# Performance work log

Hardware: AMD Instinct MI355X
Metric: run time of the kernel (lower is better)

The kernel has to match this reference:

```python
import jax, jax.numpy as jnp
import numpy as np

N_NODES = 1024
BATCH = 64
IN_CH = 12        # history steps = GAT feature dim = LSTM sequence length
N_PRED = 12
HEADS = 8
E = 1048576       # edges in the batched graph (avg degree 16)
N = BATCH * N_NODES
K = N_NODES * N_PRED
H1, H2 = 32, 128  # lstm hidden sizes


def setup_inputs() -> dict:
    key = jax.random.key(0)
    ks = jax.random.split(key, 16)
    s = 0.05
    f32 = jnp.float32
    return {
        "x": jax.random.normal(ks[0], (N, IN_CH), f32),
        "edge_index": jax.random.randint(ks[1], (2, E), 0, N, jnp.int32),
        # GATConv params (concat=False -> head-mean, bias of size out_channels)
        "gat_W": jax.random.normal(ks[2], (HEADS * IN_CH, IN_CH), f32) * s,
        "att_src": jax.random.normal(ks[3], (HEADS, IN_CH), f32) * s,
        "att_dst": jax.random.normal(ks[4], (HEADS, IN_CH), f32) * s,
        "gat_bias": jnp.zeros((IN_CH,), f32),
        # LSTM1: input_size = n_nodes, hidden 32 (PyTorch gate order i,f,g,o)
        "lstm1_Wih": jax.random.normal(ks[5], (4 * H1, N_NODES), f32) * s,
        "lstm1_Whh": jax.random.normal(ks[6], (4 * H1, H1), f32) * s,
        "lstm1_bih": jnp.zeros((4 * H1,), f32),
        "lstm1_bhh": jnp.zeros((4 * H1,), f32),
        # LSTM2: input 32 -> hidden 128
        "lstm2_Wih": jax.random.normal(ks[7], (4 * H2, H1), f32) * s,
        "lstm2_Whh": jax.random.normal(ks[8], (4 * H2, H2), f32) * s,
        "lstm2_bih": jnp.zeros((4 * H2,), f32),
        "lstm2_bhh": jnp.zeros((4 * H2,), f32),
        # MLP head
        "lin1_W": jax.random.normal(ks[9], (K // 2, H2), f32) * s,
        "lin1_b": jnp.zeros((K // 2,), f32),
        "lin2_W": jax.random.normal(ks[10], (K, K // 2), f32) * s,
        "lin2_b": jnp.zeros((K,), f32),
    }


def _lstm(xs, Wih, Whh, bih, bhh, hid):
    # xs: [T, B, in]; returns all hidden states [T, B, hid]
    B = xs.shape[1]
    h0 = jnp.zeros((B, hid), xs.dtype)
    c0 = jnp.zeros((B, hid), xs.dtype)

    def step(carry, xt):
        h, c = carry
        g = xt @ Wih.T + h @ Whh.T + bih + bhh
        i, f, gg, o = jnp.split(g, 4, axis=-1)
        c = jax.nn.sigmoid(f) * c + jax.nn.sigmoid(i) * jnp.tanh(gg)
        h = jax.nn.sigmoid(o) * jnp.tanh(c)
        return (h, c), h

    _, ys = jax.lax.scan(step, (h0, c0), xs)
    return ys


def reference(x, edge_index, gat_W, att_src, att_dst, gat_bias,
              lstm1_Wih, lstm1_Whh, lstm1_bih, lstm1_bhh,
              lstm2_Wih, lstm2_Whh, lstm2_bih, lstm2_bhh,
              lin1_W, lin1_b, lin2_W, lin2_b):
    # ---- GATConv (heads=8, concat=False -> mean over heads) ----
    h = (x @ gat_W.T).reshape(N, HEADS, IN_CH)            # [N,H,C]
    loops = jnp.arange(N, dtype=edge_index.dtype)          # add self-loops (PyG default)
    src = jnp.concatenate([edge_index[0], loops])
    dst = jnp.concatenate([edge_index[1], loops])
    a_src = (h * att_src).sum(-1)                          # [N,H]
    a_dst = (h * att_dst).sum(-1)                          # [N,H]
    e = jax.nn.leaky_relu(a_src[src] + a_dst[dst], 0.2)    # [E+N,H]
    m = jax.ops.segment_max(e, dst, num_segments=N)        # scatter-softmax per dst node
    ex = jnp.exp(e - m[dst])
    denom = jax.ops.segment_sum(ex, dst, num_segments=N)
    alpha = ex / (denom[dst] + 1e-16)
    agg = jax.ops.segment_sum(alpha[:, :, None] * h[src], dst, num_segments=N)  # [N,H,C]
    g = agg.mean(axis=1) + gat_bias                        # [N,C]

    # ---- reshape: features become time axis ----
    seq = g.reshape(BATCH, N_NODES, IN_CH).transpose(2, 0, 1)  # [T=C, B, n_nodes]

    y1 = _lstm(seq, lstm1_Wih, lstm1_Whh, lstm1_bih, lstm1_bhh, H1)
    y2 = _lstm(y1, lstm2_Wih, lstm2_Whh, lstm2_bih, lstm2_bhh, H2)
    last = y2[-1]                                          # [B, H2]

    o = last @ lin1_W.T + lin1_b
    o = o @ lin2_W.T + lin2_b
    return o.reshape(BATCH, N_NODES, N_PRED)
```

## Files before the change

### kernel.cpp

```cpp
#include <hip/hip_runtime.h>
#include <math.h>

#define NNODES 65536
#define CH 12
#define NHEADS 8
#define NEDGE 1048576
#define NITEMS (NEDGE + NNODES)
#define NBATCH 64
#define TSTEPS 12

__global__ __launch_bounds__(128) void gat_prep(
    const float* __restrict__ W, const float* __restrict__ as,
    const float* __restrict__ ad, float* __restrict__ uv) {
  int t = threadIdx.x;
  if (t < 96) {
    int h = t / 12, k = t % 12;
    float su = 0.f, sv = 0.f;
#pragma unroll
    for (int c = 0; c < 12; c++) {
      float w = W[(h * 12 + c) * 12 + k];
      su += as[h * 12 + c] * w;
      sv += ad[h * 12 + c] * w;
    }
    uv[t] = su; uv[96 + t] = sv;
  }
}

__global__ __launch_bounds__(256) void gat_node2(
    const float* __restrict__ x, const float* __restrict__ uv,
    float* __restrict__ a_src, float* __restrict__ a_dst) {
  __shared__ float su[96], sv[96];
  int tid = threadIdx.x;
  if (tid < 96) { su[tid] = uv[tid]; sv[tid] = uv[96 + tid]; }
  __syncthreads();
  int n = blockIdx.x * 256 + tid;
  const float4* xp = (const float4*)(x + (size_t)n * 12);
  float4 x0 = xp[0], x1 = xp[1], x2 = xp[2];
  float xv[12] = {x0.x,x0.y,x0.z,x0.w,x1.x,x1.y,x1.z,x1.w,x2.x,x2.y,x2.z,x2.w};
  float as[8], ad[8];
#pragma unroll
  for (int h = 0; h < 8; h++) {
    float s1 = 0.f, s2 = 0.f;
#pragma unroll
    for (int k = 0; k < 12; k++) { s1 += su[h*12+k]*xv[k]; s2 += sv[h*12+k]*xv[k]; }
    as[h] = s1; ad[h] = s2;
  }
  float4* ap = (float4*)(a_src + (size_t)n * 8);
  float4* dp = (float4*)(a_dst + (size_t)n * 8);
  ap[0] = make_float4(as[0],as[1],as[2],as[3]);
  ap[1] = make_float4(as[4],as[5],as[6],as[7]);
  dp[0] = make_float4(ad[0],ad[1],ad[2],ad[3]);
  dp[1] = make_float4(ad[4],ad[5],ad[6],ad[7]);
}

__global__ __launch_bounds__(256) void csr_count(const int* __restrict__ ei,
                                                 int* __restrict__ counts) {
  int e = blockIdx.x * 256 + threadIdx.x;
  if (e >= NITEMS) return;
  int d = (e < NEDGE) ? ei[NEDGE + e] : (e - NEDGE);
  atomicAdd(&counts[d], 1);
}

__global__ __launch_bounds__(1024) void csr_scan(const int* __restrict__ counts,
                                                 int* __restrict__ offsets,
                                                 int* __restrict__ cursor) {
  __shared__ int part[1024];
  int t = threadIdx.x;
  int base = t * 64;
  int s = 0;
  for (int i = 0; i < 64; i++) s += counts[base + i];
  part[t] = s;
  __syncthreads();
  for (int off = 1; off < 1024; off <<= 1) {
    int v = (t >= off) ? part[t - off] : 0;
    __syncthreads();
    part[t] += v;
    __syncthreads();
  }
  int run = (t == 0) ? 0 : part[t - 1];
  for (int i = 0; i < 64; i++) {
    offsets[base + i] = run;
    cursor[base + i] = run;
    run += counts[base + i];
  }
}

__global__ __launch_bounds__(256) void csr_scatter(const int* __restrict__ ei,
                                                   int* __restrict__ cursor,
                                                   int* __restrict__ csr) {
  int e = blockIdx.x * 256 + threadIdx.x;
  if (e >= NITEMS) return;
  int s, d;
  if (e < NEDGE) { s = ei[e]; d = ei[NEDGE + e]; } else { s = d = e - NEDGE; }
  int pos = atomicAdd(&cursor[d], 1);
  csr[pos] = s;
}

__global__ __launch_bounds__(256) void gat_agg(
    const int* __restrict__ offsets, const int* __restrict__ counts,
    const int* __restrict__ csr, const float* __restrict__ a_src,
    const float* __restrict__ a_dst, const float* __restrict__ x,
    const float* __restrict__ gat_W, const float* __restrict__ gat_bias,
    float* __restrict__ gT) {
  __shared__ float sW[1152];
  __shared__ float sB[12];
  int tid = threadIdx.x;
  for (int i = tid; i < 1152; i += 256) sW[i] = gat_W[i];
  if (tid < 12) sB[tid] = gat_bias[tid];
  __syncthreads();
  int gid = blockIdx.x * 256 + tid;
  int d = gid >> 3, h = gid & 7;
  int start = offsets[d], deg = counts[d];
  float adh = a_dst[(size_t)d * 8 + h];
  float denom = 0.f;
  for (int i = 0; i < deg; i++) {
    int s = csr[start + i];
    float e = a_src[(size_t)s * 8 + h] + adh;
    e = e > 0.f ? e : 0.2f * e;
    denom += expf(e);
  }
  float inv = 1.f / (denom + 1e-16f);
  float acc[12];
#pragma unroll
  for (int c = 0; c < 12; c++) acc[c] = 0.f;
  for (int i = 0; i < deg; i++) {
    int s = csr[start + i];
    float e = a_src[(size_t)s * 8 + h] + adh;
    e = e > 0.f ? e : 0.2f * e;
    float al = expf(e) * inv;
    const float4* xp = (const float4*)(x + (size_t)s * 12);
    float4 x0 = xp[0], x1 = xp[1], x2 = xp[2];
    acc[0] += al*x0.x; acc[1] += al*x0.y; acc[2]  += al*x0.z; acc[3]  += al*x0.w;
    acc[4] += al*x1.x; acc[5] += al*x1.y; acc[6]  += al*x1.z; acc[7]  += al*x1.w;
    acc[8] += al*x2.x; acc[9] += al*x2.y; acc[10] += al*x2.z; acc[11] += al*x2.w;
  }
  float y[12];
#pragma unroll
  for (int c = 0; c < 12; c++) {
    const float* wr = sW + (h * 12 + c) * 12;
    float t = 0.f;
#pragma unroll
    for (int k = 0; k < 12; k++) t += wr[k] * acc[k];
    y[c] = t;
  }
#pragma unroll
  for (int off = 1; off < 8; off <<= 1) {
#pragma unroll
    for (int c = 0; c < 12; c++) y[c] += __shfl_xor(y[c], off);
  }
  if (h == 0) {
    int b = d >> 10, np = d & 1023;
#pragma unroll
    for (int t = 0; t < 12; t++)
      gT[((size_t)(t * 64 + b)) * 1024 + np] = y[t] * 0.125f + sB[t];
  }
}

template <bool ATOMIC>
__global__ __launch_bounds__(256) void gemm_bt(
    const float* __restrict__ A, const float* __restrict__ B,
    const float* __restrict__ bias0, const float* __restrict__ bias1,
    float* __restrict__ C, int M, int N, int K, int kLen) {
  __shared__ float As[16][68];
  __shared__ float Bs[16][68];
  int m0 = blockIdx.y * 64, n0 = blockIdx.x * 64;
  int k0 = blockIdx.z * kLen;
  int tid = threadIdx.x;
  int lr = tid >> 2, lq = tid & 3;
  int tn = tid & 15, tm = tid >> 4;
  float acc[4][4];
#pragma unroll
  for (int i = 0; i < 4; i++)
#pragma unroll
    for (int j = 0; j < 4; j++) acc[i][j] = 0.f;

  for (int kk = 0; kk < kLen; kk += 16) {
    float4 a4 = *(const float4*)(A + (size_t)(m0 + lr) * K + k0 + kk + lq * 4);
    float4 b4 = *(const float4*)(B + (size_t)(n0 + lr) * K + k0 + kk + lq * 4);
    As[lq * 4 + 0][lr] = a4.x; As[lq * 4 + 1][lr] = a4.y;
    As[lq * 4 + 2][lr] = a4.z; As[lq * 4 + 3][lr] = a4.w;
    Bs[lq * 4 + 0][lr] = b4.x; Bs[lq * 4 + 1][lr] = b4.y;
    Bs[lq * 4 + 2][lr] = b4.z; Bs[lq * 4 + 3][lr] = b4.w;
    __syncthreads();
#pragma unroll
    for (int k = 0; k < 16; k++) {
      float4 av = *(const float4*)(&As[k][tm * 4]);
      float4 bv = *(const float4*)(&Bs[k][tn * 4]);
      acc[0][0] += av.x * bv.x; acc[0][1] += av.x * bv.y; acc[0][2] += av.x * bv.z; acc[0][3] += av.x * bv.w;
      acc[1][0] += av.y * bv.x; acc[1][1] += av.y * bv.y; acc[1][2] += av.y * bv.z; acc[1][3] += av.y * bv.w;
      acc[2][0] += av.z * bv.x; acc[2][1] += av.z * bv.y; acc[2][2] += av.z * bv.z; acc[2][3] += av.z * bv.w;
      acc[3][0] += av.w * bv.x; acc[3][1] += av.w * bv.y; acc[3][2] += av.w * bv.z; acc[3][3] += av.w * bv.w;
    }
    __syncthreads();
  }
#pragma unroll
  for (int i = 0; i < 4; i++) {
    int m = m0 + tm * 4 + i;
#pragma unroll
    for (int j = 0; j < 4; j++) {
      int n = n0 + tn * 4 + j;
      float v = acc[i][j];
      if (ATOMIC) {
        atomicAdd(&C[(size_t)m * N + n], v);
      } else {
        v += bias0[n];
        if (bias1) v += bias1[n];
        C[(size_t)m * N + n] = v;
      }
    }
  }
}

__global__ __launch_bounds__(128) void lstm1_scan(
    const float* __restrict__ X1, const float* __restrict__ Whh,
    float* __restrict__ y1) {
  __shared__ float sW[128 * 33];
  __shared__ float sh[32];
  __shared__ float sg[128];
  int b = blockIdx.x, g = threadIdx.x;
  for (int i = g; i < 128 * 32; i += 128) { int r = i >> 5, c = i & 31; sW[r * 33 + c] = Whh[i]; }
  if (g < 32) sh[g] = 0.f;
  float cst = 0.f;
  __syncthreads();
  for (int t = 0; t < TSTEPS; t++) {
    float acc = X1[(size_t)(t * 64 + b) * 128 + g];
#pragma unroll
    for (int k = 0; k < 32; k++) acc += sh[k] * sW[g * 33 + k];
    sg[g] = acc;
    __syncthreads();
    if (g < 32) {
      float iv = sg[g], fv = sg[32 + g], gv = sg[64 + g], ov = sg[96 + g];
      float si = 1.f / (1.f + expf(-iv));
      float sf = 1.f / (1.f + expf(-fv));
      float so = 1.f / (1.f + expf(-ov));
      cst = sf * cst + si * tanhf(gv);
      float hn = so * tanhf(cst);
      sh[g] = hn;
      y1[(size_t)(t * 64 + b) * 32 + g] = hn;
    }
    __syncthreads();
  }
}

__global__ __launch_bounds__(512) void lstm2_scan(
    const float* __restrict__ X2, const float* __restrict__ Whh,
    float* __restrict__ h2) {
  __shared__ float sh[128];
  __shared__ float sg[512];
  int b = blockIdx.x, g = threadIdx.x;
  if (g < 128) sh[g] = 0.f;
  float cst = 0.f;
  __syncthreads();
  const float4* wp = (const float4*)(Whh + (size_t)g * 128);
  for (int t = 0; t < TSTEPS; t++) {
    float acc = X2[(size_t)(t * 64 + b) * 512 + g];
#pragma unroll 8
    for (int q = 0; q < 32; q++) {
      float4 w = wp[q];
      acc += sh[q * 4 + 0] * w.x + sh[q * 4 + 1] * w.y +
             sh[q * 4 + 2] * w.z + sh[q * 4 + 3] * w.w;
    }
    sg[g] = acc;
    __syncthreads();
    if (g < 128) {
      float iv = sg[g], fv = sg[128 + g], gv = sg[256 + g], ov = sg[384 + g];
      float si = 1.f / (1.f + expf(-iv));
      float sf = 1.f / (1.f + expf(-fv));
      float so = 1.f / (1.f + expf(-ov));
      cst = sf * cst + si * tanhf(gv);
      float hn = so * tanhf(cst);
      sh[g] = hn;
      if (t == TSTEPS - 1) h2[(size_t)b * 128 + g] = hn;
    }
    __syncthreads();
  }
}

__global__ __launch_bounds__(256) void out_init(float* __restrict__ out,
                                                const float* __restrict__ bias) {
  int i = blockIdx.x * 256 + threadIdx.x;
  if (i >= NBATCH * 12288) return;
  out[i] = bias[i % 12288];
}

extern "C" void kernel_launch(void* const* d_in, const int* in_sizes, int n_in,
                              void* d_out, int out_size, void* d_ws, size_t ws_size,
                              hipStream_t stream) {
  const float* x        = (const float*)d_in[0];
  const int*   ei       = (const int*)d_in[1];
  const float* gat_W    = (const float*)d_in[2];
  const float* att_src  = (const float*)d_in[3];
  const float* att_dst  = (const float*)d_in[4];
  const float* gat_bias = (const float*)d_in[5];
  const float* l1_Wih   = (const float*)d_in[6];
  const float* l1_Whh   = (const float*)d_in[7];
  const float* l1_bih   = (const float*)d_in[8];
  const float* l1_bhh   = (const float*)d_in[9];
  const float* l2_Wih   = (const float*)d_in[10];
  const float* l2_Whh   = (const float*)d_in[11];
  const float* l2_bih   = (const float*)d_in[12];
  const float* l2_bhh   = (const float*)d_in[13];
  const float* lin1_W   = (const float*)d_in[14];
  const float* lin1_b   = (const float*)d_in[15];
  const float* lin2_W   = (const float*)d_in[16];
  const float* lin2_b   = (const float*)d_in[17];
  float* out = (float*)d_out;

  float* ws    = (float*)d_ws;
  float* a_src = ws;
  float* a_dst = a_src + 524288;
  float* uv    = a_dst + 524288;
  float* gT    = uv + 256;
  float* X1    = gT + 786432;
  float* y1    = X1 + 98304;
  float* X2    = y1 + 24576;
  float* h2    = X2 + 393216;
  float* o1    = h2 + 8192;
  int* counts  = (int*)(o1 + 393216);
  int* offsets = counts + 65536;
  int* cursor  = offsets + 65536;
  int* csr     = cursor + 65536;

  hipMemsetAsync(counts, 0, 65536 * sizeof(int), stream);

  gat_prep<<<1, 128, 0, stream>>>(gat_W, att_src, att_dst, uv);
  gat_node2<<<NNODES / 256, 256, 0, stream>>>(x, uv, a_src, a_dst);
  csr_count<<<(NITEMS + 255) / 256, 256, 0, stream>>>(ei, counts);
  csr_scan<<<1, 1024, 0, stream>>>(counts, offsets, cursor);
  csr_scatter<<<(NITEMS + 255) / 256, 256, 0, stream>>>(ei, cursor, csr);
  gat_agg<<<NNODES * 8 / 256, 256, 0, stream>>>(offsets, counts, csr, a_src,
                                                a_dst, x, gat_W, gat_bias, gT);

  {
    dim3 g(128 / 64, 768 / 64, 1);
    gemm_bt<false><<<g, 256, 0, stream>>>(gT, l1_Wih, l1_bih, l1_bhh, X1, 768, 128, 1024, 1024);
  }
  lstm1_scan<<<64, 128, 0, stream>>>(X1, l1_Whh, y1);

  {
    dim3 g(512 / 64, 768 / 64, 1);
    gemm_bt<false><<<g, 256, 0, stream>>>(y1, l2_Wih, l2_bih, l2_bhh, X2, 768, 512, 32, 32);
  }
  lstm2_scan<<<64, 512, 0, stream>>>(X2, l2_Whh, h2);

  {
    dim3 g(6144 / 64, 64 / 64, 1);
    gemm_bt<false><<<g, 256, 0, stream>>>(h2, lin1_W, lin1_b, nullptr, o1, 64, 6144, 128, 128);
  }

  out_init<<<NBATCH * 12288 / 256, 256, 0, stream>>>(out, lin2_b);
  {
    dim3 g(12288 / 64, 64 / 64, 4);
    gemm_bt<true><<<g, 256, 0, stream>>>(o1, lin2_W, nullptr, nullptr, out, 64, 12288, 6144, 6144 / 4);
  }
}
```

Measured before the change: 912.2 us.

## Parallelize GAT edges per wave, prefetch GEMM tiles, and split-K more GEMMs

The GAT aggregation now gives each destination node a full 64-lane wave, with 8 lanes per head striding over edges and shuffle reductions, in place of one thread per (node, head) walking all edges serially. The GEMM kernel register-prefetches the next K-slice of A and B while computing on the current one. The LSTM1 input projection becomes an 8-way split-K atomic GEMM over a bias-initialized buffer, and the final linear layer's split-K goes from 4 to 16 to fill more CUs. The extra atomics and the bias-init launch add traffic and make the summation order nondeterministic.

```diff
diff --git a/kernel.cpp b/kernel.cpp
--- a/kernel.cpp
+++ b/kernel.cpp
@@ -108,22 +108,26 @@
   for (int i = tid; i < 1152; i += 256) sW[i] = gat_W[i];
   if (tid < 12) sB[tid] = gat_bias[tid];
   __syncthreads();
-  int gid = blockIdx.x * 256 + tid;
-  int d = gid >> 3, h = gid & 7;
+  int wave = tid >> 6, lane = tid & 63;
+  int d = blockIdx.x * 4 + wave;
+  int h = lane & 7, sub = lane >> 3;
   int start = offsets[d], deg = counts[d];
   float adh = a_dst[(size_t)d * 8 + h];
   float denom = 0.f;
-  for (int i = 0; i < deg; i++) {
+  for (int i = sub; i < deg; i += 8) {
     int s = csr[start + i];
     float e = a_src[(size_t)s * 8 + h] + adh;
     e = e > 0.f ? e : 0.2f * e;
     denom += expf(e);
   }
+  denom += __shfl_xor(denom, 8);
+  denom += __shfl_xor(denom, 16);
+  denom += __shfl_xor(denom, 32);
   float inv = 1.f / (denom + 1e-16f);
   float acc[12];
 #pragma unroll
   for (int c = 0; c < 12; c++) acc[c] = 0.f;
-  for (int i = 0; i < deg; i++) {
+  for (int i = sub; i < deg; i += 8) {
     int s = csr[start + i];
     float e = a_src[(size_t)s * 8 + h] + adh;
     e = e > 0.f ? e : 0.2f * e;
@@ -144,11 +148,11 @@
     y[c] = t;
   }
 #pragma unroll
-  for (int off = 1; off < 8; off <<= 1) {
+  for (int off = 1; off < 64; off <<= 1) {
 #pragma unroll
     for (int c = 0; c < 12; c++) y[c] += __shfl_xor(y[c], off);
   }
-  if (h == 0) {
+  if (lane == 0) {
     int b = d >> 10, np = d & 1023;
 #pragma unroll
     for (int t = 0; t < 12; t++)
@@ -174,14 +178,22 @@
 #pragma unroll
     for (int j = 0; j < 4; j++) acc[i][j] = 0.f;
 
+  const float* Ap = A + (size_t)(m0 + lr) * K + k0 + lq * 4;
+  const float* Bp = B + (size_t)(n0 + lr) * K + k0 + lq * 4;
+  float4 a4 = *(const float4*)Ap;
+  float4 b4 = *(const float4*)Bp;
+
   for (int kk = 0; kk < kLen; kk += 16) {
-    float4 a4 = *(const float4*)(A + (size_t)(m0 + lr) * K + k0 + kk + lq * 4);
-    float4 b4 = *(const float4*)(B + (size_t)(n0 + lr) * K + k0 + kk + lq * 4);
     As[lq * 4 + 0][lr] = a4.x; As[lq * 4 + 1][lr] = a4.y;
     As[lq * 4 + 2][lr] = a4.z; As[lq * 4 + 3][lr] = a4.w;
     Bs[lq * 4 + 0][lr] = b4.x; Bs[lq * 4 + 1][lr] = b4.y;
     Bs[lq * 4 + 2][lr] = b4.z; Bs[lq * 4 + 3][lr] = b4.w;
     __syncthreads();
+    float4 a4n, b4n;
+    if (kk + 16 < kLen) {
+      a4n = *(const float4*)(Ap + kk + 16);
+      b4n = *(const float4*)(Bp + kk + 16);
+    }
 #pragma unroll
     for (int k = 0; k < 16; k++) {
       float4 av = *(const float4*)(&As[k][tm * 4]);
@@ -192,6 +204,7 @@
       acc[3][0] += av.w * bv.x; acc[3][1] += av.w * bv.y; acc[3][2] += av.w * bv.z; acc[3][3] += av.w * bv.w;
     }
     __syncthreads();
+    a4 = a4n; b4 = b4n;
   }
 #pragma unroll
   for (int i = 0; i < 4; i++) {
@@ -211,6 +224,17 @@
   }
 }
 
+__global__ __launch_bounds__(256) void init_bias2(
+    float* __restrict__ C, const float* __restrict__ b0,
+    const float* __restrict__ b1, int total, int N) {
+  int i = blockIdx.x * 256 + threadIdx.x;
+  if (i >= total) return;
+  int n = i % N;
+  float v = b0[n];
+  if (b1) v += b1[n];
+  C[i] = v;
+}
+
 __global__ __launch_bounds__(128) void lstm1_scan(
     const float* __restrict__ X1, const float* __restrict__ Whh,
     float* __restrict__ y1) {
@@ -274,13 +298,6 @@
     }
     __syncthreads();
   }
-}
-
-__global__ __launch_bounds__(256) void out_init(float* __restrict__ out,
-                                                const float* __restrict__ bias) {
-  int i = blockIdx.x * 256 + threadIdx.x;
-  if (i >= NBATCH * 12288) return;
-  out[i] = bias[i % 12288];
 }
 
 extern "C" void kernel_launch(void* const* d_in, const int* in_sizes, int n_in,
@@ -328,12 +345,13 @@
   csr_count<<<(NITEMS + 255) / 256, 256, 0, stream>>>(ei, counts);
   csr_scan<<<1, 1024, 0, stream>>>(counts, offsets, cursor);
   csr_scatter<<<(NITEMS + 255) / 256, 256, 0, stream>>>(ei, cursor, csr);
-  gat_agg<<<NNODES * 8 / 256, 256, 0, stream>>>(offsets, counts, csr, a_src,
-                                                a_dst, x, gat_W, gat_bias, gT);
-
+  gat_agg<<<NNODES / 4, 256, 0, stream>>>(offsets, counts, csr, a_src,
+                                          a_dst, x, gat_W, gat_bias, gT);
+
+  init_bias2<<<(768 * 128 + 255) / 256, 256, 0, stream>>>(X1, l1_bih, l1_bhh, 768 * 128, 128);
   {
-    dim3 g(128 / 64, 768 / 64, 1);
-    gemm_bt<false><<<g, 256, 0, stream>>>(gT, l1_Wih, l1_bih, l1_bhh, X1, 768, 128, 1024, 1024);
+    dim3 g(128 / 64, 768 / 64, 8);
+    gemm_bt<true><<<g, 256, 0, stream>>>(gT, l1_Wih, nullptr, nullptr, X1, 768, 128, 1024, 1024 / 8);
   }
   lstm1_scan<<<64, 128, 0, stream>>>(X1, l1_Whh, y1);
 
@@ -348,9 +366,9 @@
     gemm_bt<false><<<g, 256, 0, stream>>>(h2, lin1_W, lin1_b, nullptr, o1, 64, 6144, 128, 128);
   }
 
-  out_init<<<NBATCH * 12288 / 256, 256, 0, stream>>>(out, lin2_b);
+  init_bias2<<<(NBATCH * 12288 + 255) / 256, 256, 0, stream>>>(out, lin2_b, nullptr, NBATCH * 12288, 12288);
   {
-    dim3 g(12288 / 64, 64 / 64, 4);
-    gemm_bt<true><<<g, 256, 0, stream>>>(o1, lin2_W, nullptr, nullptr, out, 64, 12288, 6144, 6144 / 4);
-  }
-}
+    dim3 g(12288 / 64, 64 / 64, 16);
+    gemm_bt<true><<<g, 256, 0, stream>>>(o1, lin2_W, nullptr, nullptr, out, 64, 12288, 6144, 6144 / 16);
+  }
+}
```

Result: slower. 957.9 us (+5.0%).
